# Optimization experiments

Measured on AMD Instinct MI355X. Metric: run time of the kernel, lower is better.

Reference implementation:

```python
import jax, jax.numpy as jnp
import numpy as np

PARENTS = [-1,0,0,0,1,2,3,4,5,6,7,8,9,9,9,12,13,14,16,17,18,19,20,21]
B, J, IN_DIM, H, HEADS, OUT_DIM, L = 16384, 24, 3, 128, 4, 6, 3
C = H // HEADS  # 32 per-head channels
SLOPE = 0.2     # PyG GATConv leaky_relu negative slope


def _edges():
    # skeleton edges (both directions) + self loops (PyG add_self_loops=True)
    e = []
    for c, p in enumerate(PARENTS):
        if p >= 0:
            e.append((p, c)); e.append((c, p))
    for j in range(len(PARENTS)):
        e.append((j, j))
    a = np.asarray(e, dtype=np.int32)
    return a[:, 0], a[:, 1]


def _ln(x, g, b, eps=1e-5):
    m = jnp.mean(x, axis=-1, keepdims=True)
    v = jnp.var(x, axis=-1, keepdims=True)
    return (x - m) * jax.lax.rsqrt(v + eps) * g + b


def setup_inputs() -> dict:
    key = jax.random.key(0)
    ks = jax.random.split(key, 12)
    s = 0.05
    src_np, dst_np = _edges()
    return {
        "x": jax.random.normal(ks[0], (B, J, IN_DIM), jnp.float32),
        "in_w": jax.random.normal(ks[1], (IN_DIM, H), jnp.float32) * s,
        "in_b": jnp.zeros((H,), jnp.float32),
        "res_w": jax.random.normal(ks[2], (IN_DIM, H), jnp.float32) * s,
        "res_b": jnp.zeros((H,), jnp.float32),
        "pos": jax.random.normal(ks[3], (J, H), jnp.float32) * s,
        "gat_w": jax.random.normal(ks[4], (L, H, H), jnp.float32) * s,
        "att_s": jax.random.normal(ks[5], (L, HEADS, C), jnp.float32) * s,
        "att_d": jax.random.normal(ks[6], (L, HEADS, C), jnp.float32) * s,
        "gat_b": jnp.zeros((L, H), jnp.float32),
        "ln_g": jnp.ones((L, H), jnp.float32),
        "ln_b": jnp.zeros((L, H), jnp.float32),
        "w1": jax.random.normal(ks[7], (H, H // 2), jnp.float32) * s,
        "b1": jnp.zeros((H // 2,), jnp.float32),
        "lng2": jnp.ones((H // 2,), jnp.float32),
        "lnb2": jnp.zeros((H // 2,), jnp.float32),
        "w2": jax.random.normal(ks[8], (H // 2, OUT_DIM), jnp.float32) * s,
        "b2": jnp.zeros((OUT_DIM,), jnp.float32),
        "src": jnp.asarray(src_np),
        "dst": jnp.asarray(dst_np),
    }


def reference(x, in_w, in_b, res_w, res_b, pos, gat_w, att_s, att_d, gat_b,
              ln_g, ln_b, w1, b1, lng2, lnb2, w2, b2, src, dst):
    h = x @ in_w + in_b + pos[None]                     # [B,J,H]
    res = x @ res_w + res_b                             # [B,J,H]
    for l in range(L):
        hp = h
        xl = (h @ gat_w[l]).reshape(B, J, HEADS, C)     # [B,J,heads,C]
        a_s = jnp.einsum('bjhc,hc->bjh', xl, att_s[l])
        a_d = jnp.einsum('bjhc,hc->bjh', xl, att_d[l])
        e = jax.nn.leaky_relu(a_s[:, src] + a_d[:, dst], SLOPE)   # [B,E,heads]
        # scatter-softmax over incoming edges per destination joint
        m = jnp.full((B, J, HEADS), -1e9, e.dtype).at[:, dst].max(e)
        p = jnp.exp(e - m[:, dst])
        den = jnp.zeros((B, J, HEADS), e.dtype).at[:, dst].add(p)
        alpha = p / den[:, dst]                          # [B,E,heads]
        msg = xl[:, src] * alpha[..., None]              # [B,E,heads,C]
        out = jnp.zeros_like(xl).at[:, dst].add(msg).reshape(B, J, H) + gat_b[l]
        out = _ln(jax.nn.elu(out), ln_g[l], ln_b[l])
        h = out + hp if l > 0 else out
    h = h + res
    y = jax.nn.relu(h @ w1 + b1)
    y = _ln(y, lng2, lnb2)
    return y @ w2 + b2                                   # [B,J,6]
```

## Files before the change

### kernel.cpp

```cpp
#include <hip/hip_runtime.h>


#define J 24
#define ROWS 48
#define HB 136
#define YS 68

typedef __attribute__((ext_vector_type(8))) short short8;
typedef __attribute__((ext_vector_type(4))) float f32x4;

__device__ unsigned short g_wt[64512];

__constant__ int c_deg[J] = {4,3,3,3,3,3,3,3,3,5,2,2,3,3,3,2,3,3,3,3,3,3,2,2};
__constant__ int c_inc[J][5] = {
  {1,2,3,0,0},{0,4,1,0,0},{0,5,2,0,0},{0,6,3,0,0},{1,7,4,0,0},{2,8,5,0,0},
  {3,9,6,0,0},{4,10,7,0,0},{5,11,8,0,0},{6,12,13,14,9},{7,10,0,0,0},{8,11,0,0,0},
  {9,15,12,0,0},{9,16,13,0,0},{9,17,14,0,0},{12,15,0,0,0},{13,18,16,0,0},{14,19,17,0,0},
  {16,20,18,0,0},{17,21,19,0,0},{18,22,20,0,0},{19,23,21,0,0},{20,22,0,0,0},{21,23,0,0,0}
};

__device__ __forceinline__ unsigned short f2bf(float f) {
  unsigned u = __builtin_bit_cast(unsigned, f);
  u = (u + 0x7FFFu + ((u >> 16) & 1u)) >> 16;
  return (unsigned short)u;
}
__device__ __forceinline__ float bf2f(unsigned short u) {
  return __builtin_bit_cast(float, (unsigned)u << 16);
}

__global__ __launch_bounds__(256) void prep_weights(
    const float* __restrict__ gat_w, const float* __restrict__ att_s,
    const float* __restrict__ att_d, const float* __restrict__ w1,
    const float* __restrict__ w2)
{
  const int idx = blockIdx.x * 256 + threadIdx.x;
  if (idx < 49152) {
    const int l = idx >> 14, rem = idx & 16383, n = rem >> 7, k = rem & 127;
    g_wt[idx] = f2bf(gat_w[l*16384 + k*128 + n]);
  } else if (idx < 57344) {
    const int i2 = idx - 49152, m = i2 >> 7, k = i2 & 127;
    g_wt[idx] = f2bf(w1[k*64 + m]);
  } else if (idx < 63488) {
    const int i2 = idx - 57344;
    const int l = i2 >> 11, r = i2 & 2047, j = r >> 7, k = r & 127;
    float v = 0.f;
    if (j < 8) {
      const int sd = j >> 2, hhh = j & 3;
      const float* av = (sd ? att_d : att_s) + (l*4 + hhh)*32;
      const float* wp = gat_w + l*16384 + k*128 + hhh*32;
#pragma unroll 8
      for (int c = 0; c < 32; ++c) v += wp[c] * av[c];
    }
    g_wt[idx] = f2bf(v);
  } else if (idx < 64512) {
    const int i2 = idx - 63488, o = i2 >> 6, m = i2 & 63;
    g_wt[idx] = f2bf(o < 6 ? w2[m*6 + o] : 0.f);
  }
}

__global__ __launch_bounds__(64) void gat_fused(
    const float* __restrict__ x,     const float* __restrict__ in_w,  const float* __restrict__ in_b,
    const float* __restrict__ res_w, const float* __restrict__ res_b, const float* __restrict__ pos,
    const float* __restrict__ gat_b, const float* __restrict__ ln_g,  const float* __restrict__ ln_b,
    const float* __restrict__ b1,    const float* __restrict__ lng2,  const float* __restrict__ lnb2,
    const float* __restrict__ b2,    float* __restrict__ out)
{
  __shared__ __align__(16) unsigned short s_hb [ROWS*HB];
  __shared__ __align__(16) unsigned short s_xlb[ROWS*HB];
  __shared__ float s_x[144];
  __shared__ float s_asd[ROWS*8];
  __shared__ float s_alp[ROWS*20];

  const int tid = threadIdx.x;
  const long blk = blockIdx.x;
  const int l16 = tid & 15, q = tid >> 4;
  const int g = tid >> 3, c8 = tid & 7, cb = c8*16, hh = c8 >> 1;

  {
    const float* xb = x + blk*144;
    s_x[tid]      = xb[tid];
    s_x[64 + tid] = xb[64 + tid];
    if (tid < 16) s_x[128 + tid] = xb[128 + tid];
  }
  __syncthreads();

#pragma unroll
  for (int i = 0; i < 6; ++i) {
    const int r = g + 8*i;
    const int bp = (i < 3) ? 0 : 1;
    const int j = r - 24*bp;
    const float x0 = s_x[bp*72 + j*3], x1 = s_x[bp*72 + j*3 + 1], x2 = s_x[bp*72 + j*3 + 2];
    short8 p0, p1;
#pragma unroll
    for (int c4 = 0; c4 < 4; ++c4) {
      const float4 w0 = *(const float4*)&in_w[      cb + c4*4];
      const float4 w1v= *(const float4*)&in_w[128 + cb + c4*4];
      const float4 w2v= *(const float4*)&in_w[256 + cb + c4*4];
      const float4 bb = *(const float4*)&in_b[      cb + c4*4];
      const float4 pp = *(const float4*)&pos[j*128 + cb + c4*4];
      float v[4];
      v[0] = x0*w0.x + x1*w1v.x + x2*w2v.x + bb.x + pp.x;
      v[1] = x0*w0.y + x1*w1v.y + x2*w2v.y + bb.y + pp.y;
      v[2] = x0*w0.z + x1*w1v.z + x2*w2v.z + bb.z + pp.z;
      v[3] = x0*w0.w + x1*w1v.w + x2*w2v.w + bb.w + pp.w;
#pragma unroll
      for (int cc = 0; cc < 4; ++cc) {
        const int c = c4*4 + cc;
        if (c < 8) p0[c] = (short)f2bf(v[cc]); else p1[c-8] = (short)f2bf(v[cc]);
      }
    }
    *(short8*)&s_hb[r*HB + cb]     = p0;
    *(short8*)&s_hb[r*HB + cb + 8] = p1;
  }
  __syncthreads();

  for (int l = 0; l < 3; ++l) {
    {
      const unsigned short* Wl = &g_wt[l*16384];
      short8 af[3][4];
#pragma unroll
      for (int t = 0; t < 3; ++t)
#pragma unroll
        for (int ks = 0; ks < 4; ++ks)
          af[t][ks] = *(const short8*)&s_hb[(t*16 + l16)*HB + ks*32 + q*8];

#pragma unroll
      for (int nt = 0; nt < 8; ++nt) {
        f32x4 acc[3] = { {0,0,0,0}, {0,0,0,0}, {0,0,0,0} };
#pragma unroll
        for (int ks = 0; ks < 4; ++ks) {
          const short8 bfr = *(const short8*)&Wl[(nt*16 + l16)*128 + ks*32 + q*8];
#pragma unroll
          for (int t = 0; t < 3; ++t)
            acc[t] = __builtin_amdgcn_mfma_f32_16x16x32_bf16(af[t][ks], bfr, acc[t], 0, 0, 0);
        }
        const int col = nt*16 + l16;
#pragma unroll
        for (int t = 0; t < 3; ++t)
#pragma unroll
          for (int r4 = 0; r4 < 4; ++r4)
            s_xlb[(t*16 + q*4 + r4)*HB + col] = f2bf(acc[t][r4]);
      }
      const unsigned short* Wa = &g_wt[57344 + l*2048];
      f32x4 la[3] = { {0,0,0,0}, {0,0,0,0}, {0,0,0,0} };
#pragma unroll
      for (int ks = 0; ks < 4; ++ks) {
        const short8 ba = *(const short8*)&Wa[l16*128 + ks*32 + q*8];
#pragma unroll
        for (int t = 0; t < 3; ++t)
          la[t] = __builtin_amdgcn_mfma_f32_16x16x32_bf16(af[t][ks], ba, la[t], 0, 0, 0);
      }
      if (l16 < 8) {
#pragma unroll
        for (int t = 0; t < 3; ++t)
#pragma unroll
          for (int r4 = 0; r4 < 4; ++r4)
            s_asd[(t*16 + q*4 + r4)*8 + l16] = la[t][r4];
      }
    }
    __syncthreads();

#pragma unroll
    for (int it = 0; it < 3; ++it) {
      const int item = tid + it*64;
      const int r = item >> 2, hh2 = item & 3;
      const int base = (r >= 24) ? 24 : 0, j = r - base;
      const int dg = c_deg[j];
      const float ad = s_asd[r*8 + 4 + hh2];
      float ev[5];
      float m = -1e30f;
#pragma unroll
      for (int e = 0; e < 5; ++e) if (e < dg) {
        float ee = s_asd[(base + c_inc[j][e])*8 + hh2] + ad;
        ee = (ee >= 0.f) ? ee : 0.2f*ee;
        ev[e] = ee;
        m = fmaxf(m, ee);
      }
      float den = 0.f;
#pragma unroll
      for (int e = 0; e < 5; ++e) if (e < dg) { ev[e] = __expf(ev[e]-m); den += ev[e]; }
      const float inv = 1.f/den;
#pragma unroll
      for (int e = 0; e < 5; ++e) if (e < dg) s_alp[(r*5+e)*4 + hh2] = ev[e]*inv;
    }
    __syncthreads();

#pragma unroll
    for (int i = 0; i < 6; ++i) {
      const int r = g + 8*i;
      const int bp = (i < 3) ? 0 : 1;
      const int base = 24*bp, j = r - base;
      const int dg = c_deg[j];
      float ov[16];
#pragma unroll
      for (int c4 = 0; c4 < 4; ++c4) {
        const float4 gb4 = *(const float4*)&gat_b[l*128 + cb + c4*4];
        ov[c4*4+0]=gb4.x; ov[c4*4+1]=gb4.y; ov[c4*4+2]=gb4.z; ov[c4*4+3]=gb4.w;
      }
#pragma unroll
      for (int e = 0; e < 5; ++e) if (e < dg) {
        const float al = s_alp[(r*5+e)*4 + hh];
        const unsigned short* xp = &s_xlb[(base + c_inc[j][e])*HB + cb];
        const short8 xa = *(const short8*)xp;
        const short8 xb = *(const short8*)(xp + 8);
#pragma unroll
        for (int c = 0; c < 8; ++c) {
          ov[c]   += al * bf2f((unsigned short)xa[c]);
          ov[8+c] += al * bf2f((unsigned short)xb[c]);
        }
      }
      float s = 0.f, s2 = 0.f;
#pragma unroll
      for (int c = 0; c < 16; ++c) {
        float v = ov[c];
        v = (v > 0.f) ? v : (__expf(v) - 1.f);
        ov[c] = v;
        s += v; s2 += v*v;
      }
#pragma unroll
      for (int off = 1; off < 8; off <<= 1) {
        s  += __shfl_xor(s,  off, 64);
        s2 += __shfl_xor(s2, off, 64);
      }
      const float mean = s * (1.f/128.f);
      const float rstd = rsqrtf(s2 * (1.f/128.f) - mean*mean + 1e-5f);

      float hp[16];
      if (l > 0) {
        const unsigned short* hpp = &s_hb[r*HB + cb];
        const short8 ha = *(const short8*)hpp;
        const short8 hb2 = *(const short8*)(hpp + 8);
#pragma unroll
        for (int c = 0; c < 8; ++c) { hp[c] = bf2f((unsigned short)ha[c]); hp[8+c] = bf2f((unsigned short)hb2[c]); }
      }

      short8 p0, p1;
      if (l == 2) {
        const float x0 = s_x[bp*72 + j*3], x1 = s_x[bp*72 + j*3 + 1], x2 = s_x[bp*72 + j*3 + 2];
#pragma unroll
        for (int c4 = 0; c4 < 4; ++c4) {
          const float4 lg4 = *(const float4*)&ln_g[l*128 + cb + c4*4];
          const float4 lb4 = *(const float4*)&ln_b[l*128 + cb + c4*4];
          const float4 rw0 = *(const float4*)&res_w[      cb + c4*4];
          const float4 rw1 = *(const float4*)&res_w[128 + cb + c4*4];
          const float4 rw2 = *(const float4*)&res_w[256 + cb + c4*4];
          const float4 rb4 = *(const float4*)&res_b[      cb + c4*4];
          const float lgv[4] = {lg4.x, lg4.y, lg4.z, lg4.w};
          const float lbv[4] = {lb4.x, lb4.y, lb4.z, lb4.w};
          const float r0[4]  = {rw0.x, rw0.y, rw0.z, rw0.w};
          const float r1[4]  = {rw1.x, rw1.y, rw1.z, rw1.w};
          const float r2[4]  = {rw2.x, rw2.y, rw2.z, rw2.w};
          const float rb[4]  = {rb4.x, rb4.y, rb4.z, rb4.w};
#pragma unroll
          for (int cc = 0; cc < 4; ++cc) {
            const int c = c4*4 + cc;
            float v = (ov[c]-mean)*rstd*lgv[cc] + lbv[cc] + hp[c];
            v += x0*r0[cc] + x1*r1[cc] + x2*r2[cc] + rb[cc];
            if (c < 8) p0[c] = (short)f2bf(v); else p1[c-8] = (short)f2bf(v);
          }
        }
      } else {
#pragma unroll
        for (int c4 = 0; c4 < 4; ++c4) {
          const float4 lg4 = *(const float4*)&ln_g[l*128 + cb + c4*4];
          const float4 lb4 = *(const float4*)&ln_b[l*128 + cb + c4*4];
          const float lgv[4] = {lg4.x, lg4.y, lg4.z, lg4.w};
          const float lbv[4] = {lb4.x, lb4.y, lb4.z, lb4.w};
#pragma unroll
          for (int cc = 0; cc < 4; ++cc) {
            const int c = c4*4 + cc;
            float v = (ov[c]-mean)*rstd*lgv[cc] + lbv[cc];
            if (l > 0) v += hp[c];
            if (c < 8) p0[c] = (short)f2bf(v); else p1[c-8] = (short)f2bf(v);
          }
        }
      }
      *(short8*)&s_hb[r*HB + cb]     = p0;
      *(short8*)&s_hb[r*HB + cb + 8] = p1;
    }
    __syncthreads();
  }

  {
    const unsigned short* W1 = &g_wt[49152];
    float* s_y = (float*)s_xlb;
    short8 af[3][4];
#pragma unroll
    for (int t = 0; t < 3; ++t)
#pragma unroll
      for (int ks = 0; ks < 4; ++ks)
        af[t][ks] = *(const short8*)&s_hb[(t*16 + l16)*HB + ks*32 + q*8];
#pragma unroll
    for (int nt = 0; nt < 4; ++nt) {
      const float bv = b1[nt*16 + l16];
      f32x4 acc[3] = { {bv,bv,bv,bv}, {bv,bv,bv,bv}, {bv,bv,bv,bv} };
#pragma unroll
      for (int ks = 0; ks < 4; ++ks) {
        const short8 bfr = *(const short8*)&W1[(nt*16 + l16)*128 + ks*32 + q*8];
#pragma unroll
        for (int t = 0; t < 3; ++t)
          acc[t] = __builtin_amdgcn_mfma_f32_16x16x32_bf16(af[t][ks], bfr, acc[t], 0, 0, 0);
      }
      const int col = nt*16 + l16;
#pragma unroll
      for (int t = 0; t < 3; ++t)
#pragma unroll
        for (int r4 = 0; r4 < 4; ++r4)
          s_y[(t*16 + q*4 + r4)*YS + col] = fmaxf(acc[t][r4], 0.f);
    }
  }
  __syncthreads();

#pragma unroll
  for (int it = 0; it < 2; ++it) {
    const int item = tid + it*64;
    if (item < 96) {
      const int row = item >> 1, half = item & 1;
      const float* yr = (const float*)s_xlb + row*YS + half*32;
      float yv[32];
      float s = 0.f, s2 = 0.f;
#pragma unroll
      for (int c4 = 0; c4 < 8; ++c4) {
        const float4 v4 = *(const float4*)&yr[c4*4];
        yv[c4*4+0]=v4.x; yv[c4*4+1]=v4.y; yv[c4*4+2]=v4.z; yv[c4*4+3]=v4.w;
        s += v4.x+v4.y+v4.z+v4.w;
        s2 += v4.x*v4.x + v4.y*v4.y + v4.z*v4.z + v4.w*v4.w;
      }
      s  += __shfl_xor(s,  1, 64);
      s2 += __shfl_xor(s2, 1, 64);
      const float mean = s * (1.f/64.f);
      const float rstd = rsqrtf(s2 * (1.f/64.f) - mean*mean + 1e-5f);
      short8 pk[4];
#pragma unroll
      for (int c = 0; c < 32; ++c) {
        const int m = half*32 + c;
        const float yl = (yv[c]-mean)*rstd*lng2[m] + lnb2[m];
        pk[c >> 3][c & 7] = (short)f2bf(yl);
      }
#pragma unroll
      for (int p = 0; p < 4; ++p)
        *(short8*)&s_hb[row*HB + half*32 + p*8] = pk[p];
    }
  }
  __syncthreads();

  {
    const unsigned short* W2 = &g_wt[63488];
    const short8 bf0 = *(const short8*)&W2[l16*64 + q*8];
    const short8 bf1 = *(const short8*)&W2[l16*64 + 32 + q*8];
    const float bv = (l16 < 6) ? b2[l16] : 0.f;
#pragma unroll
    for (int t = 0; t < 3; ++t) {
      f32x4 acc = {0,0,0,0};
      const short8 a0 = *(const short8*)&s_hb[(t*16 + l16)*HB + q*8];
      acc = __builtin_amdgcn_mfma_f32_16x16x32_bf16(a0, bf0, acc, 0, 0, 0);
      const short8 a1 = *(const short8*)&s_hb[(t*16 + l16)*HB + 32 + q*8];
      acc = __builtin_amdgcn_mfma_f32_16x16x32_bf16(a1, bf1, acc, 0, 0, 0);
      if (l16 < 6) {
#pragma unroll
        for (int r4 = 0; r4 < 4; ++r4) {
          const int row = t*16 + q*4 + r4;
          const int bp = (row >= 24) ? 1 : 0;
          const int jj = row - 24*bp;
          out[(blk*2 + bp)*144 + jj*6 + l16] = acc[r4] + bv;
        }
      }
    }
  }
}

extern "C" void kernel_launch(void* const* d_in, const int* in_sizes, int n_in,
                              void* d_out, int out_size, void* d_ws, size_t ws_size,
                              hipStream_t stream) {
  (void)n_in; (void)out_size; (void)d_ws; (void)ws_size;
  const float* x     = (const float*)d_in[0];
  const float* in_w  = (const float*)d_in[1];
  const float* in_b  = (const float*)d_in[2];
  const float* res_w = (const float*)d_in[3];
  const float* res_b = (const float*)d_in[4];
  const float* pos   = (const float*)d_in[5];
  const float* gat_w = (const float*)d_in[6];
  const float* att_s = (const float*)d_in[7];
  const float* att_d = (const float*)d_in[8];
  const float* gat_b = (const float*)d_in[9];
  const float* ln_g  = (const float*)d_in[10];
  const float* ln_b  = (const float*)d_in[11];
  const float* w1    = (const float*)d_in[12];
  const float* b1    = (const float*)d_in[13];
  const float* lng2  = (const float*)d_in[14];
  const float* lnb2  = (const float*)d_in[15];
  const float* w2    = (const float*)d_in[16];
  const float* b2    = (const float*)d_in[17];
  float* out = (float*)d_out;

  const int B = in_sizes[0] / (J*3);
  hipLaunchKernelGGL(prep_weights, dim3((64512 + 255)/256), dim3(256), 0, stream,
                     gat_w, att_s, att_d, w1, w2);
  hipLaunchKernelGGL(gat_fused, dim3(B/2), dim3(64), 0, stream,
                     x, in_w, in_b, res_w, res_b, pos, gat_b, ln_g, ln_b,
                     b1, lng2, lnb2, b2, out);
}
```

Baseline: 572.0 us.

## Fuse softmax into aggregation, transpose MFMA outputs for vector stores, pack adjacency

Computes the per-destination attention softmax inside the aggregation loop instead of in a separate pass, which removes the s_alp shared buffer and one barrier per layer. It swaps the MFMA operand order so each lane holds consecutive output columns, allowing packed bf16x2 and float4 shared and global stores in place of scalar ones. It packs degree and neighbour indices into a single constant word per joint and disables unrolling on several loops to reduce code size and register pressure. In exchange, the softmax is recomputed for each of the 8 channel-group threads per row, and the rolled loops lose some instruction-level parallelism.

```diff
diff --git a/kernel.cpp b/kernel.cpp
--- a/kernel.cpp
+++ b/kernel.cpp
@@ -11,18 +11,27 @@
 
 __device__ unsigned short g_wt[64512];
 
-__constant__ int c_deg[J] = {4,3,3,3,3,3,3,3,3,5,2,2,3,3,3,2,3,3,3,3,3,3,2,2};
-__constant__ int c_inc[J][5] = {
-  {1,2,3,0,0},{0,4,1,0,0},{0,5,2,0,0},{0,6,3,0,0},{1,7,4,0,0},{2,8,5,0,0},
-  {3,9,6,0,0},{4,10,7,0,0},{5,11,8,0,0},{6,12,13,14,9},{7,10,0,0,0},{8,11,0,0,0},
-  {9,15,12,0,0},{9,16,13,0,0},{9,17,14,0,0},{12,15,0,0,0},{13,18,16,0,0},{14,19,17,0,0},
-  {16,20,18,0,0},{17,21,19,0,0},{18,22,20,0,0},{19,23,21,0,0},{20,22,0,0,0},{21,23,0,0,0}
+#define PK5(d,a,b,c,e,f) ((unsigned)(d)|((unsigned)(a)<<3)|((unsigned)(b)<<8)|((unsigned)(c)<<13)|((unsigned)(e)<<18)|((unsigned)(f)<<23))
+__constant__ unsigned c_pack[J] = {
+  PK5(4,1,2,3,0,0),  PK5(3,0,4,1,0,0),  PK5(3,0,5,2,0,0),  PK5(3,0,6,3,0,0),
+  PK5(3,1,7,4,0,0),  PK5(3,2,8,5,0,0),  PK5(3,3,9,6,0,0),  PK5(3,4,10,7,0,0),
+  PK5(3,5,11,8,0,0), PK5(5,6,12,13,14,9),PK5(2,7,10,0,0,0), PK5(2,8,11,0,0,0),
+  PK5(3,9,15,12,0,0),PK5(3,9,16,13,0,0),PK5(3,9,17,14,0,0),PK5(2,12,15,0,0,0),
+  PK5(3,13,18,16,0,0),PK5(3,14,19,17,0,0),PK5(3,16,20,18,0,0),PK5(3,17,21,19,0,0),
+  PK5(3,18,22,20,0,0),PK5(3,19,23,21,0,0),PK5(2,20,22,0,0,0),PK5(2,21,23,0,0,0)
 };
 
 __device__ __forceinline__ unsigned short f2bf(float f) {
   unsigned u = __builtin_bit_cast(unsigned, f);
   u = (u + 0x7FFFu + ((u >> 16) & 1u)) >> 16;
   return (unsigned short)u;
+}
+__device__ __forceinline__ unsigned pack2bf(float a, float b) {
+  unsigned ua = __builtin_bit_cast(unsigned, a);
+  unsigned ub = __builtin_bit_cast(unsigned, b);
+  ua = (ua + 0x7FFFu + ((ua >> 16) & 1u)) >> 16;
+  ub = (ub + 0x7FFFu + ((ub >> 16) & 1u)) & 0xFFFF0000u;
+  return ua | ub;
 }
 __device__ __forceinline__ float bf2f(unsigned short u) {
   return __builtin_bit_cast(float, (unsigned)u << 16);
@@ -69,7 +78,6 @@
   __shared__ __align__(16) unsigned short s_xlb[ROWS*HB];
   __shared__ float s_x[144];
   __shared__ float s_asd[ROWS*8];
-  __shared__ float s_alp[ROWS*20];
 
   const int tid = threadIdx.x;
   const long blk = blockIdx.x;
@@ -84,13 +92,13 @@
   }
   __syncthreads();
 
-#pragma unroll
+#pragma unroll 1
   for (int i = 0; i < 6; ++i) {
     const int r = g + 8*i;
-    const int bp = (i < 3) ? 0 : 1;
+    const int bp = (r >= 24) ? 1 : 0;
     const int j = r - 24*bp;
     const float x0 = s_x[bp*72 + j*3], x1 = s_x[bp*72 + j*3 + 1], x2 = s_x[bp*72 + j*3 + 2];
-    short8 p0, p1;
+    float v[16];
 #pragma unroll
     for (int c4 = 0; c4 < 4; ++c4) {
       const float4 w0 = *(const float4*)&in_w[      cb + c4*4];
@@ -98,33 +106,33 @@
       const float4 w2v= *(const float4*)&in_w[256 + cb + c4*4];
       const float4 bb = *(const float4*)&in_b[      cb + c4*4];
       const float4 pp = *(const float4*)&pos[j*128 + cb + c4*4];
-      float v[4];
-      v[0] = x0*w0.x + x1*w1v.x + x2*w2v.x + bb.x + pp.x;
-      v[1] = x0*w0.y + x1*w1v.y + x2*w2v.y + bb.y + pp.y;
-      v[2] = x0*w0.z + x1*w1v.z + x2*w2v.z + bb.z + pp.z;
-      v[3] = x0*w0.w + x1*w1v.w + x2*w2v.w + bb.w + pp.w;
-#pragma unroll
-      for (int cc = 0; cc < 4; ++cc) {
-        const int c = c4*4 + cc;
-        if (c < 8) p0[c] = (short)f2bf(v[cc]); else p1[c-8] = (short)f2bf(v[cc]);
-      }
-    }
-    *(short8*)&s_hb[r*HB + cb]     = p0;
-    *(short8*)&s_hb[r*HB + cb + 8] = p1;
+      v[c4*4+0] = x0*w0.x + x1*w1v.x + x2*w2v.x + bb.x + pp.x;
+      v[c4*4+1] = x0*w0.y + x1*w1v.y + x2*w2v.y + bb.y + pp.y;
+      v[c4*4+2] = x0*w0.z + x1*w1v.z + x2*w2v.z + bb.z + pp.z;
+      v[c4*4+3] = x0*w0.w + x1*w1v.w + x2*w2v.w + bb.w + pp.w;
+    }
+    uint4 pk0, pk1;
+    pk0.x = pack2bf(v[0],v[1]);   pk0.y = pack2bf(v[2],v[3]);
+    pk0.z = pack2bf(v[4],v[5]);   pk0.w = pack2bf(v[6],v[7]);
+    pk1.x = pack2bf(v[8],v[9]);   pk1.y = pack2bf(v[10],v[11]);
+    pk1.z = pack2bf(v[12],v[13]); pk1.w = pack2bf(v[14],v[15]);
+    *(uint4*)&s_hb[r*HB + cb]     = pk0;
+    *(uint4*)&s_hb[r*HB + cb + 8] = pk1;
   }
   __syncthreads();
 
+#pragma unroll 1
   for (int l = 0; l < 3; ++l) {
+    short8 af[3][4];
+#pragma unroll
+    for (int t = 0; t < 3; ++t)
+#pragma unroll
+      for (int ks = 0; ks < 4; ++ks)
+        af[t][ks] = *(const short8*)&s_hb[(t*16 + l16)*HB + ks*32 + q*8];
+
     {
       const unsigned short* Wl = &g_wt[l*16384];
-      short8 af[3][4];
-#pragma unroll
-      for (int t = 0; t < 3; ++t)
-#pragma unroll
-        for (int ks = 0; ks < 4; ++ks)
-          af[t][ks] = *(const short8*)&s_hb[(t*16 + l16)*HB + ks*32 + q*8];
-
-#pragma unroll
+#pragma unroll 1
       for (int nt = 0; nt < 8; ++nt) {
         f32x4 acc[3] = { {0,0,0,0}, {0,0,0,0}, {0,0,0,0} };
 #pragma unroll
@@ -132,14 +140,15 @@
           const short8 bfr = *(const short8*)&Wl[(nt*16 + l16)*128 + ks*32 + q*8];
 #pragma unroll
           for (int t = 0; t < 3; ++t)
-            acc[t] = __builtin_amdgcn_mfma_f32_16x16x32_bf16(af[t][ks], bfr, acc[t], 0, 0, 0);
-        }
-        const int col = nt*16 + l16;
-#pragma unroll
-        for (int t = 0; t < 3; ++t)
-#pragma unroll
-          for (int r4 = 0; r4 < 4; ++r4)
-            s_xlb[(t*16 + q*4 + r4)*HB + col] = f2bf(acc[t][r4]);
+            acc[t] = __builtin_amdgcn_mfma_f32_16x16x32_bf16(bfr, af[t][ks], acc[t], 0, 0, 0);
+        }
+#pragma unroll
+        for (int t = 0; t < 3; ++t) {
+          uint2 w;
+          w.x = pack2bf(acc[t][0], acc[t][1]);
+          w.y = pack2bf(acc[t][2], acc[t][3]);
+          *(uint2*)&s_xlb[(t*16 + l16)*HB + nt*16 + q*4] = w;
+        }
       }
       const unsigned short* Wa = &g_wt[57344 + l*2048];
       f32x4 la[3] = { {0,0,0,0}, {0,0,0,0}, {0,0,0,0} };
@@ -148,49 +157,43 @@
         const short8 ba = *(const short8*)&Wa[l16*128 + ks*32 + q*8];
 #pragma unroll
         for (int t = 0; t < 3; ++t)
-          la[t] = __builtin_amdgcn_mfma_f32_16x16x32_bf16(af[t][ks], ba, la[t], 0, 0, 0);
-      }
-      if (l16 < 8) {
-#pragma unroll
-        for (int t = 0; t < 3; ++t)
-#pragma unroll
-          for (int r4 = 0; r4 < 4; ++r4)
-            s_asd[(t*16 + q*4 + r4)*8 + l16] = la[t][r4];
+          la[t] = __builtin_amdgcn_mfma_f32_16x16x32_bf16(ba, af[t][ks], la[t], 0, 0, 0);
+      }
+      if (q < 2) {
+#pragma unroll
+        for (int t = 0; t < 3; ++t) {
+          float4 w; w.x = la[t][0]; w.y = la[t][1]; w.z = la[t][2]; w.w = la[t][3];
+          *(float4*)&s_asd[(t*16 + l16)*8 + q*4] = w;
+        }
       }
     }
     __syncthreads();
 
-#pragma unroll
-    for (int it = 0; it < 3; ++it) {
-      const int item = tid + it*64;
-      const int r = item >> 2, hh2 = item & 3;
-      const int base = (r >= 24) ? 24 : 0, j = r - base;
-      const int dg = c_deg[j];
-      const float ad = s_asd[r*8 + 4 + hh2];
-      float ev[5];
-      float m = -1e30f;
-#pragma unroll
-      for (int e = 0; e < 5; ++e) if (e < dg) {
-        float ee = s_asd[(base + c_inc[j][e])*8 + hh2] + ad;
-        ee = (ee >= 0.f) ? ee : 0.2f*ee;
-        ev[e] = ee;
-        m = fmaxf(m, ee);
-      }
-      float den = 0.f;
-#pragma unroll
-      for (int e = 0; e < 5; ++e) if (e < dg) { ev[e] = __expf(ev[e]-m); den += ev[e]; }
-      const float inv = 1.f/den;
-#pragma unroll
-      for (int e = 0; e < 5; ++e) if (e < dg) s_alp[(r*5+e)*4 + hh2] = ev[e]*inv;
-    }
-    __syncthreads();
-
-#pragma unroll
+#pragma unroll 1
     for (int i = 0; i < 6; ++i) {
       const int r = g + 8*i;
-      const int bp = (i < 3) ? 0 : 1;
+      const int bp = (r >= 24) ? 1 : 0;
       const int base = 24*bp, j = r - base;
-      const int dg = c_deg[j];
+      const unsigned pkw = c_pack[j];
+      const int dg = pkw & 7;
+      const unsigned pp = pkw >> 3;
+
+      const float ad = s_asd[r*8 + 4 + hh];
+      float al[5];
+      float mx = -1e30f;
+#pragma unroll
+      for (int e = 0; e < 5; ++e) if (e < dg) {
+        const int src = (pp >> (5*e)) & 31;
+        float ee = s_asd[(base + src)*8 + hh] + ad;
+        ee = (ee >= 0.f) ? ee : 0.2f*ee;
+        al[e] = ee;
+        mx = fmaxf(mx, ee);
+      }
+      float den = 0.f;
+#pragma unroll
+      for (int e = 0; e < 5; ++e) if (e < dg) { al[e] = __expf(al[e]-mx); den += al[e]; }
+      const float inv = 1.f/den;
+
       float ov[16];
 #pragma unroll
       for (int c4 = 0; c4 < 4; ++c4) {
@@ -199,14 +202,15 @@
       }
 #pragma unroll
       for (int e = 0; e < 5; ++e) if (e < dg) {
-        const float al = s_alp[(r*5+e)*4 + hh];
-        const unsigned short* xp = &s_xlb[(base + c_inc[j][e])*HB + cb];
+        const float a = al[e]*inv;
+        const int src = (pp >> (5*e)) & 31;
+        const unsigned short* xp = &s_xlb[(base + src)*HB + cb];
         const short8 xa = *(const short8*)xp;
         const short8 xb = *(const short8*)(xp + 8);
 #pragma unroll
         for (int c = 0; c < 8; ++c) {
-          ov[c]   += al * bf2f((unsigned short)xa[c]);
-          ov[8+c] += al * bf2f((unsigned short)xb[c]);
+          ov[c]   += a * bf2f((unsigned short)xa[c]);
+          ov[8+c] += a * bf2f((unsigned short)xb[c]);
         }
       }
       float s = 0.f, s2 = 0.f;
@@ -226,7 +230,7 @@
       const float rstd = rsqrtf(s2 * (1.f/128.f) - mean*mean + 1e-5f);
 
       float hp[16];
-      if (l > 0) {
+      {
         const unsigned short* hpp = &s_hb[r*HB + cb];
         const short8 ha = *(const short8*)hpp;
         const short8 hb2 = *(const short8*)(hpp + 8);
@@ -234,49 +238,41 @@
         for (int c = 0; c < 8; ++c) { hp[c] = bf2f((unsigned short)ha[c]); hp[8+c] = bf2f((unsigned short)hb2[c]); }
       }
 
-      short8 p0, p1;
+#pragma unroll
+      for (int c4 = 0; c4 < 4; ++c4) {
+        const float4 lg4 = *(const float4*)&ln_g[l*128 + cb + c4*4];
+        const float4 lb4 = *(const float4*)&ln_b[l*128 + cb + c4*4];
+        const float lgv[4] = {lg4.x, lg4.y, lg4.z, lg4.w};
+        const float lbv[4] = {lb4.x, lb4.y, lb4.z, lb4.w};
+#pragma unroll
+        for (int cc = 0; cc < 4; ++cc) {
+          const int c = c4*4 + cc;
+          float v = (ov[c]-mean)*rstd*lgv[cc] + lbv[cc];
+          if (l > 0) v += hp[c];
+          ov[c] = v;
+        }
+      }
       if (l == 2) {
         const float x0 = s_x[bp*72 + j*3], x1 = s_x[bp*72 + j*3 + 1], x2 = s_x[bp*72 + j*3 + 2];
 #pragma unroll
         for (int c4 = 0; c4 < 4; ++c4) {
-          const float4 lg4 = *(const float4*)&ln_g[l*128 + cb + c4*4];
-          const float4 lb4 = *(const float4*)&ln_b[l*128 + cb + c4*4];
           const float4 rw0 = *(const float4*)&res_w[      cb + c4*4];
           const float4 rw1 = *(const float4*)&res_w[128 + cb + c4*4];
           const float4 rw2 = *(const float4*)&res_w[256 + cb + c4*4];
           const float4 rb4 = *(const float4*)&res_b[      cb + c4*4];
-          const float lgv[4] = {lg4.x, lg4.y, lg4.z, lg4.w};
-          const float lbv[4] = {lb4.x, lb4.y, lb4.z, lb4.w};
-          const float r0[4]  = {rw0.x, rw0.y, rw0.z, rw0.w};
-          const float r1[4]  = {rw1.x, rw1.y, rw1.z, rw1.w};
-          const float r2[4]  = {rw2.x, rw2.y, rw2.z, rw2.w};
-          const float rb[4]  = {rb4.x, rb4.y, rb4.z, rb4.w};
-#pragma unroll
-          for (int cc = 0; cc < 4; ++cc) {
-            const int c = c4*4 + cc;
-            float v = (ov[c]-mean)*rstd*lgv[cc] + lbv[cc] + hp[c];
-            v += x0*r0[cc] + x1*r1[cc] + x2*r2[cc] + rb[cc];
-            if (c < 8) p0[c] = (short)f2bf(v); else p1[c-8] = (short)f2bf(v);
-          }
-        }
-      } else {
-#pragma unroll
-        for (int c4 = 0; c4 < 4; ++c4) {
-          const float4 lg4 = *(const float4*)&ln_g[l*128 + cb + c4*4];
-          const float4 lb4 = *(const float4*)&ln_b[l*128 + cb + c4*4];
-          const float lgv[4] = {lg4.x, lg4.y, lg4.z, lg4.w};
-          const float lbv[4] = {lb4.x, lb4.y, lb4.z, lb4.w};
-#pragma unroll
-          for (int cc = 0; cc < 4; ++cc) {
-            const int c = c4*4 + cc;
-            float v = (ov[c]-mean)*rstd*lgv[cc] + lbv[cc];
-            if (l > 0) v += hp[c];
-            if (c < 8) p0[c] = (short)f2bf(v); else p1[c-8] = (short)f2bf(v);
-          }
-        }
-      }
-      *(short8*)&s_hb[r*HB + cb]     = p0;
-      *(short8*)&s_hb[r*HB + cb + 8] = p1;
+          ov[c4*4+0] += x0*rw0.x + x1*rw1.x + x2*rw2.x + rb4.x;
+          ov[c4*4+1] += x0*rw0.y + x1*rw1.y + x2*rw2.y + rb4.y;
+          ov[c4*4+2] += x0*rw0.z + x1*rw1.z + x2*rw2.z + rb4.z;
+          ov[c4*4+3] += x0*rw0.w + x1*rw1.w + x2*rw2.w + rb4.w;
+        }
+      }
+      uint4 pk0, pk1;
+      pk0.x = pack2bf(ov[0],ov[1]);   pk0.y = pack2bf(ov[2],ov[3]);
+      pk0.z = pack2bf(ov[4],ov[5]);   pk0.w = pack2bf(ov[6],ov[7]);
+      pk1.x = pack2bf(ov[8],ov[9]);   pk1.y = pack2bf(ov[10],ov[11]);
+      pk1.z = pack2bf(ov[12],ov[13]); pk1.w = pack2bf(ov[14],ov[15]);
+      *(uint4*)&s_hb[r*HB + cb]     = pk0;
+      *(uint4*)&s_hb[r*HB + cb + 8] = pk1;
     }
     __syncthreads();
   }
@@ -290,28 +286,31 @@
 #pragma unroll
       for (int ks = 0; ks < 4; ++ks)
         af[t][ks] = *(const short8*)&s_hb[(t*16 + l16)*HB + ks*32 + q*8];
-#pragma unroll
+#pragma unroll 1
     for (int nt = 0; nt < 4; ++nt) {
-      const float bv = b1[nt*16 + l16];
-      f32x4 acc[3] = { {bv,bv,bv,bv}, {bv,bv,bv,bv}, {bv,bv,bv,bv} };
+      const float4 b1v = *(const float4*)&b1[nt*16 + q*4];
+      f32x4 acc[3];
+#pragma unroll
+      for (int t = 0; t < 3; ++t) { acc[t][0]=b1v.x; acc[t][1]=b1v.y; acc[t][2]=b1v.z; acc[t][3]=b1v.w; }
 #pragma unroll
       for (int ks = 0; ks < 4; ++ks) {
         const short8 bfr = *(const short8*)&W1[(nt*16 + l16)*128 + ks*32 + q*8];
 #pragma unroll
         for (int t = 0; t < 3; ++t)
-          acc[t] = __builtin_amdgcn_mfma_f32_16x16x32_bf16(af[t][ks], bfr, acc[t], 0, 0, 0);
-      }
-      const int col = nt*16 + l16;
-#pragma unroll
-      for (int t = 0; t < 3; ++t)
-#pragma unroll
-        for (int r4 = 0; r4 < 4; ++r4)
-          s_y[(t*16 + q*4 + r4)*YS + col] = fmaxf(acc[t][r4], 0.f);
+          acc[t] = __builtin_amdgcn_mfma_f32_16x16x32_bf16(bfr, af[t][ks], acc[t], 0, 0, 0);
+      }
+#pragma unroll
+      for (int t = 0; t < 3; ++t) {
+        float4 w;
+        w.x = fmaxf(acc[t][0], 0.f); w.y = fmaxf(acc[t][1], 0.f);
+        w.z = fmaxf(acc[t][2], 0.f); w.w = fmaxf(acc[t][3], 0.f);
+        *(float4*)&s_y[(t*16 + l16)*YS + nt*16 + q*4] = w;
+      }
     }
   }
   __syncthreads();
 
-#pragma unroll
+#pragma unroll 1
   for (int it = 0; it < 2; ++it) {
     const int item = tid + it*64;
     if (item < 96) {
@@ -330,16 +329,25 @@
       s2 += __shfl_xor(s2, 1, 64);
       const float mean = s * (1.f/64.f);
       const float rstd = rsqrtf(s2 * (1.f/64.f) - mean*mean + 1e-5f);
-      short8 pk[4];
+      float yl[32];
 #pragma unroll
       for (int c = 0; c < 32; ++c) {
         const int m = half*32 + c;
-        const float yl = (yv[c]-mean)*rstd*lng2[m] + lnb2[m];
-        pk[c >> 3][c & 7] = (short)f2bf(yl);
-      }
-#pragma unroll
-      for (int p = 0; p < 4; ++p)
-        *(short8*)&s_hb[row*HB + half*32 + p*8] = pk[p];
+        yl[c] = (yv[c]-mean)*rstd*lng2[m] + lnb2[m];
+      }
+      uint4 pkA, pkB;
+      pkA.x = pack2bf(yl[0],yl[1]);   pkA.y = pack2bf(yl[2],yl[3]);
+      pkA.z = pack2bf(yl[4],yl[5]);   pkA.w = pack2bf(yl[6],yl[7]);
+      pkB.x = pack2bf(yl[8],yl[9]);   pkB.y = pack2bf(yl[10],yl[11]);
+      pkB.z = pack2bf(yl[12],yl[13]); pkB.w = pack2bf(yl[14],yl[15]);
+      *(uint4*)&s_hb[row*HB + half*32]     = pkA;
+      *(uint4*)&s_hb[row*HB + half*32 + 8] = pkB;
+      pkA.x = pack2bf(yl[16],yl[17]); pkA.y = pack2bf(yl[18],yl[19]);
+      pkA.z = pack2bf(yl[20],yl[21]); pkA.w = pack2bf(yl[22],yl[23]);
+      pkB.x = pack2bf(yl[24],yl[25]); pkB.y = pack2bf(yl[26],yl[27]);
+      pkB.z = pack2bf(yl[28],yl[29]); pkB.w = pack2bf(yl[30],yl[31]);
+      *(uint4*)&s_hb[row*HB + half*32 + 16] = pkA;
+      *(uint4*)&s_hb[row*HB + half*32 + 24] = pkB;
     }
   }
   __syncthreads();
@@ -348,22 +356,26 @@
     const unsigned short* W2 = &g_wt[63488];
     const short8 bf0 = *(const short8*)&W2[l16*64 + q*8];
     const short8 bf1 = *(const short8*)&W2[l16*64 + 32 + q*8];
-    const float bv = (l16 < 6) ? b2[l16] : 0.f;
-#pragma unroll
+#pragma unroll 1
     for (int t = 0; t < 3; ++t) {
       f32x4 acc = {0,0,0,0};
       const short8 a0 = *(const short8*)&s_hb[(t*16 + l16)*HB + q*8];
-      acc = __builtin_amdgcn_mfma_f32_16x16x32_bf16(a0, bf0, acc, 0, 0, 0);
+      acc = __builtin_amdgcn_mfma_f32_16x16x32_bf16(bf0, a0, acc, 0, 0, 0);
       const short8 a1 = *(const short8*)&s_hb[(t*16 + l16)*HB + 32 + q*8];
-      acc = __builtin_amdgcn_mfma_f32_16x16x32_bf16(a1, bf1, acc, 0, 0, 0);
-      if (l16 < 6) {
-#pragma unroll
-        for (int r4 = 0; r4 < 4; ++r4) {
-          const int row = t*16 + q*4 + r4;
-          const int bp = (row >= 24) ? 1 : 0;
-          const int jj = row - 24*bp;
-          out[(blk*2 + bp)*144 + jj*6 + l16] = acc[r4] + bv;
-        }
+      acc = __builtin_amdgcn_mfma_f32_16x16x32_bf16(bf1, a1, acc, 0, 0, 0);
+      const int row = t*16 + l16;
+      const int bp = (row >= 24) ? 1 : 0;
+      const int jj = row - 24*bp;
+      float* op = out + (blk*2 + bp)*144 + jj*6;
+      if (q == 0) {
+        float4 w;
+        w.x = acc[0] + b2[0]; w.y = acc[1] + b2[1];
+        w.z = acc[2] + b2[2]; w.w = acc[3] + b2[3];
+        *(float4*)op = w;
+      } else if (q == 1) {
+        float2 w;
+        w.x = acc[0] + b2[4]; w.y = acc[1] + b2[5];
+        *(float2*)(op + 4) = w;
       }
     }
   }
```

Result: faster. 475.2 us (median of 2 runs) (-16.9%).
